# Kernel optimization log

Measured on AMD Instinct MI355X. Metric: run time of the kernel, lower is better.

The kernel has to match this reference:

```python
import jax, jax.numpy as jnp
import numpy as np

EPS = 1e-7  # keras.backend.epsilon()
ROUTINGS = 3


def _squash(s):
    # s: [B, k, d]; squash over last (capsule-dim) axis, matching squash(..., axis=-2)
    # applied to [B,1,k,d,1] in the original.
    ss = jnp.sum(s * s, axis=-1, keepdims=True) + EPS
    return (jnp.sqrt(ss) / (1.0 + ss)) * s


def setup_inputs() -> dict:
    key = jax.random.key(0)
    kx, kw, km = jax.random.split(key, 3)
    B, n, k, d = 32, 2048, 32, 16
    x = jax.random.normal(kx, (B, n, d), dtype=jnp.float32)
    # glorot-ish scale for W: fan ~ d
    W = jax.random.normal(kw, (1, n, k, d, d), dtype=jnp.float32) * (1.0 / np.sqrt(d))
    mu0 = jax.random.uniform(km, (B, k, d), dtype=jnp.float32)  # np.random.rand equivalent
    return {"x": x, "W": W, "mu0": mu0}


def reference(x, W, mu0):
    B, n, d = x.shape
    k = mu0.shape[1]
    pi = jnp.full((B, k), 1.0 / k, dtype=x.dtype)
    mu = mu0
    sigma = jnp.ones((B, k, d), dtype=x.dtype)
    log2pi = jnp.log(2.0 * jnp.pi).astype(x.dtype)
    R = jnp.zeros((B, n, k), dtype=x.dtype)
    for _ in range(ROUTINGS):
        # E-step: gamma[b,k,n] = pi_k * N(x_n | mu_k, diag(sigma_k^2)), normalized over k.
        z = (x[:, None, :, :] - mu[:, :, None, :]) / sigma[:, :, None, :]  # [B,k,n,d]
        logN = -0.5 * (jnp.sum(z * z, axis=-1) + d * log2pi) - jnp.sum(jnp.log(sigma), axis=-1)[:, :, None]
        gamma = jax.nn.softmax(jnp.log(pi)[:, :, None] + logN, axis=1)  # [B,k,n]
        R = jnp.transpose(gamma, (0, 2, 1))  # [B,n,k]
        # M-step
        N_k = jnp.sum(R, axis=1)  # [B,k]
        pi = N_k / n
        mu = jnp.einsum('bnk,bnd->bkd', R, x) / N_k[:, :, None]
        diff2 = (x[:, None, :, :] - mu[:, :, None, :]) ** 2  # [B,k,n,d]
        sigma = jnp.sqrt(jnp.einsum('bkn,bknd->bkd', gamma, diff2) / N_k[:, :, None])
    # caps_predicted[b,n,k,d] = W[0,n,k,d,:] @ x[b,n,:]
    caps_pred = jnp.einsum('nkde,bne->bnkd', W[0], x)
    s = jnp.sum(caps_pred * R[..., None], axis=1)  # [B,k,d]
    return _squash(s)
```

## Files before the change

kernel.cpp:

```cpp
#include <hip/hip_runtime.h>
#include <hip/hip_bf16.h>
#include <math.h>

#define BN 32
#define NN 2048
#define KK 32
#define DD 16
#define PART_C 16
#define PART_STRIDE 1056
#define SCAPS 256


typedef __attribute__((ext_vector_type(8))) short bf16x8;
typedef __attribute__((ext_vector_type(16))) float f32x16;

static __device__ __forceinline__ ushort f2bf(float f) {
    unsigned int u = __float_as_uint(f);
    return (ushort)((u + 0x7FFFu + ((u >> 16) & 1u)) >> 16);
}

template <int MODE, int FIRST>
static __device__ __forceinline__ void estep_body(
    int blk, const float* __restrict__ x, const float* __restrict__ mu0,
    const float* __restrict__ partIn, float* __restrict__ partOut,
    float* __restrict__ Rout) {
    const int b = blk >> 4;
    const int chunk = blk & 15;
    const int tid = threadIdx.x;
    const int wave = tid >> 6;
    const int lane = tid & 63;
    const int k = lane & 31;
    const int jj = lane >> 5;

    float mk[DD], ik[DD], ck;
    if (FIRST) {
        const float4* mp = (const float4*)(mu0 + (size_t)(b * KK + k) * DD);
#pragma unroll
        for (int q = 0; q < 4; q++) {
            float4 m4 = mp[q];
            mk[q*4+0]=m4.x; mk[q*4+1]=m4.y; mk[q*4+2]=m4.z; mk[q*4+3]=m4.w;
        }
#pragma unroll
        for (int d = 0; d < DD; d++) ik[d] = 1.0f;
        ck = -3.4657359028f;
    } else {
        float N = 0.f, sxv[DD], sxxv[DD];
#pragma unroll
        for (int d = 0; d < DD; d++) { sxv[d] = 0.f; sxxv[d] = 0.f; }
#pragma unroll
        for (int c = 0; c < PART_C; c++) {
            const float* base = partIn + (size_t)(b * PART_C + c) * PART_STRIDE;
            N += base[k];
#pragma unroll
            for (int d = 0; d < DD; d++) {
                sxv[d]  += base[(1 + d) * 32 + k];
                sxxv[d] += base[(17 + d) * 32 + k];
            }
        }
        float invN = 1.0f / N;
        float sumlog = 0.f;
#pragma unroll
        for (int d = 0; d < DD; d++) {
            float m_ = sxv[d] * invN;
            float v = fmaxf(sxxv[d] * invN - m_ * m_, 1e-12f);
            mk[d] = m_;
            ik[d] = rsqrtf(v);
            sumlog += __logf(v);
        }
        ck = __logf(N * (1.0f / NN)) - 0.5f * sumlog;
    }

    float aN = 0.f, aSx[DD], aSxx[DD];
#pragma unroll
    for (int d = 0; d < DD; d++) { aSx[d] = 0.f; aSxx[d] = 0.f; }

#pragma unroll 4
    for (int i = 0; i < 16; i++) {
        const int n = chunk * 128 + i * 8 + wave * 2 + jj;
        const float4* xp = (const float4*)(x + ((size_t)b * NN + n) * DD);
        float xv[DD];
#pragma unroll
        for (int q = 0; q < 4; q++) {
            float4 v = xp[q];
            xv[q*4+0]=v.x; xv[q*4+1]=v.y; xv[q*4+2]=v.z; xv[q*4+3]=v.w;
        }
        float qd = 0.f;
#pragma unroll
        for (int d = 0; d < DD; d++) {
            float z = (xv[d] - mk[d]) * ik[d];
            qd = fmaf(z, z, qd);
        }
        float logit = ck - 0.5f * qd;
        float m = logit;
#pragma unroll
        for (int off = 1; off < 32; off <<= 1) m = fmaxf(m, __shfl_xor(m, off));
        float e = __expf(logit - m);
        float ssum = e;
#pragma unroll
        for (int off = 1; off < 32; off <<= 1) ssum += __shfl_xor(ssum, off);
        float g = e / ssum;

        if (MODE == 1) {
            Rout[((size_t)b * NN + n) * KK + k] = g;
        } else {
            aN += g;
#pragma unroll
            for (int d = 0; d < DD; d++) {
                aSx[d] = fmaf(g, xv[d], aSx[d]);
                aSxx[d] = fmaf(g * xv[d], xv[d], aSxx[d]);
            }
        }
    }

    if (MODE == 0) {
        __shared__ float red[4][KK * 33];
        aN += __shfl_xor(aN, 32);
#pragma unroll
        for (int d = 0; d < DD; d++) {
            aSx[d] += __shfl_xor(aSx[d], 32);
            aSxx[d] += __shfl_xor(aSxx[d], 32);
        }
        if (jj == 0) {
            red[wave][k * 33 + 0] = aN;
#pragma unroll
            for (int d = 0; d < DD; d++) {
                red[wave][k * 33 + 1 + d] = aSx[d];
                red[wave][k * 33 + 17 + d] = aSxx[d];
            }
        }
        __syncthreads();
        float* outp = partOut + (size_t)(b * PART_C + chunk) * PART_STRIDE;
        for (int idx = tid; idx < KK * 33; idx += 256) {
            int kk = idx & 31, j = idx >> 5;
            float v = red[0][kk * 33 + j] + red[1][kk * 33 + j] +
                      red[2][kk * 33 + j] + red[3][kk * 33 + j];
            outp[idx] = v;
        }
    }
}

static __device__ __forceinline__ void xpack_body(int blk, const float* __restrict__ x,
                                                  ushort* __restrict__ xpk) {
    int idx = blk * 256 + threadIdx.x;
    int n = idx >> 6, l = idx & 63;
    int b = l & 31, e0 = (l >> 5) * 8;
    const float4* xp = (const float4*)(x + ((size_t)b * NN + n) * DD + e0);
    float4 a = xp[0], c = xp[1];
    ushort* o = xpk + (size_t)idx * 8;
    o[0]=f2bf(a.x); o[1]=f2bf(a.y); o[2]=f2bf(a.z); o[3]=f2bf(a.w);
    o[4]=f2bf(c.x); o[5]=f2bf(c.y); o[6]=f2bf(c.z); o[7]=f2bf(c.w);
}

__global__ __launch_bounds__(256, 4) void k_fused1(
    const float* __restrict__ x, const float* __restrict__ mu0,
    float* __restrict__ partOut, ushort* __restrict__ xpk) {
    if (blockIdx.x < 512)
        estep_body<0, 1>(blockIdx.x, x, mu0, nullptr, partOut, nullptr);
    else
        xpack_body(blockIdx.x - 512, x, xpk);
}

template <int MODE>
__global__ __launch_bounds__(256, 4) void k_estep(
    const float* __restrict__ x, const float* __restrict__ partIn,
    float* __restrict__ partOut, float* __restrict__ Rout) {
    estep_body<MODE, 0>(blockIdx.x, x, nullptr, partIn, partOut, Rout);
}

__global__ __launch_bounds__(256, 4) void k_caps(
    const float* __restrict__ W, const ushort* __restrict__ xpk,
    const float* __restrict__ R, float* __restrict__ s) {
    const int tid = threadIdx.x;
    const int wv = tid >> 6, l = tid & 63;
    const int chunk = blockIdx.x >> 2, tg = blockIdx.x & 3;
    const int t = tg * 4 + wv;
    const int col = l & 31, hi = l >> 5;
    const int kq = (l >> 4) & 1;
    float* sc = s + (size_t)chunk * (BN * KK * DD);

    float sacc[16];
#pragma unroll
    for (int q = 0; q < 16; q++) sacc[q] = 0.f;
    const f32x16 zacc = {0.f,0.f,0.f,0.f, 0.f,0.f,0.f,0.f,
                         0.f,0.f,0.f,0.f, 0.f,0.f,0.f,0.f};

#pragma unroll 4
    for (int i = 0; i < 8; i++) {
        const int n = chunk * 8 + i;
        bf16x8 af = *(const bf16x8*)(xpk + ((size_t)n * 64 + l) * 8);
        const float4* wp = (const float4*)(W + (((size_t)n * 512 + t * 32 + col) * DD) + hi * 8);
        float4 wlo = wp[0], whi = wp[1];
        bf16x8 bfr;
        bfr[0]=(short)f2bf(wlo.x); bfr[1]=(short)f2bf(wlo.y);
        bfr[2]=(short)f2bf(wlo.z); bfr[3]=(short)f2bf(wlo.w);
        bfr[4]=(short)f2bf(whi.x); bfr[5]=(short)f2bf(whi.y);
        bfr[6]=(short)f2bf(whi.z); bfr[7]=(short)f2bf(whi.w);
        const float* rn = R + (size_t)(4 * hi) * (NN * KK) + (size_t)n * KK + 2 * t + kq;
        float r0  = rn[(size_t) 0 * (NN * KK)];
        float r1  = rn[(size_t) 1 * (NN * KK)];
        float r2  = rn[(size_t) 2 * (NN * KK)];
        float r3  = rn[(size_t) 3 * (NN * KK)];
        float r4  = rn[(size_t) 8 * (NN * KK)];
        float r5  = rn[(size_t) 9 * (NN * KK)];
        float r6  = rn[(size_t)10 * (NN * KK)];
        float r7  = rn[(size_t)11 * (NN * KK)];
        float r8  = rn[(size_t)16 * (NN * KK)];
        float r9  = rn[(size_t)17 * (NN * KK)];
        float r10 = rn[(size_t)18 * (NN * KK)];
        float r11 = rn[(size_t)19 * (NN * KK)];
        float r12 = rn[(size_t)24 * (NN * KK)];
        float r13 = rn[(size_t)25 * (NN * KK)];
        float r14 = rn[(size_t)26 * (NN * KK)];
        float r15 = rn[(size_t)27 * (NN * KK)];

        f32x16 D = __builtin_amdgcn_mfma_f32_32x32x16_bf16(af, bfr, zacc, 0, 0, 0);

        sacc[0]  = fmaf(r0,  D[0],  sacc[0]);
        sacc[1]  = fmaf(r1,  D[1],  sacc[1]);
        sacc[2]  = fmaf(r2,  D[2],  sacc[2]);
        sacc[3]  = fmaf(r3,  D[3],  sacc[3]);
        sacc[4]  = fmaf(r4,  D[4],  sacc[4]);
        sacc[5]  = fmaf(r5,  D[5],  sacc[5]);
        sacc[6]  = fmaf(r6,  D[6],  sacc[6]);
        sacc[7]  = fmaf(r7,  D[7],  sacc[7]);
        sacc[8]  = fmaf(r8,  D[8],  sacc[8]);
        sacc[9]  = fmaf(r9,  D[9],  sacc[9]);
        sacc[10] = fmaf(r10, D[10], sacc[10]);
        sacc[11] = fmaf(r11, D[11], sacc[11]);
        sacc[12] = fmaf(r12, D[12], sacc[12]);
        sacc[13] = fmaf(r13, D[13], sacc[13]);
        sacc[14] = fmaf(r14, D[14], sacc[14]);
        sacc[15] = fmaf(r15, D[15], sacc[15]);
    }

    const int kd = t * 32 + col;
#pragma unroll
    for (int q = 0; q < 16; q++) {
        const int b = (q & 3) + 8 * (q >> 2) + 4 * hi;
        sc[(size_t)b * (KK * DD) + kd] = sacc[q];
    }
}

__global__ void k_squash(const float* __restrict__ s, float* __restrict__ out) {
    int idx = blockIdx.x * 256 + threadIdx.x;
    float v = 0.f;
#pragma unroll 8
    for (int c = 0; c < SCAPS; c++) v += s[(size_t)c * (BN * KK * DD) + idx];
    float ss = v * v;
#pragma unroll
    for (int off = 1; off < 16; off <<= 1) ss += __shfl_xor(ss, off);
    ss += 1e-7f;
    float scale = sqrtf(ss) / (1.0f + ss);
    out[idx] = v * scale;
}

extern "C" void kernel_launch(void* const* d_in, const int* in_sizes, int n_in,
                              void* d_out, int out_size, void* d_ws, size_t ws_size,
                              hipStream_t stream) {
    const float* x   = (const float*)d_in[0];
    const float* W   = (const float*)d_in[1];
    const float* mu0 = (const float*)d_in[2];
    float* ws    = (float*)d_ws;
    float* partA = ws;
    float* partB = ws + 540672;
    float* s     = ws + 1081344;
    float* R     = ws + 5275648;
    ushort* xpk  = (ushort*)(ws + 7372800);

    k_fused1<<<1024, 256, 0, stream>>>(x, mu0, partA, xpk);
    k_estep<0><<<512, 256, 0, stream>>>(x, partA, partB, nullptr);
    k_estep<1><<<512, 256, 0, stream>>>(x, partB, nullptr, R);
    k_caps<<<1024, 256, 0, stream>>>(W, xpk, R, s);
    k_squash<<<64, 256, 0, stream>>>(s, (float*)d_out);
}
```

Before: 100.4 us.

## Expand Gaussian quadratic form and give each caps wave two tiles

```diff
diff --git a/kernel.cpp b/kernel.cpp
--- a/kernel.cpp
+++ b/kernel.cpp
@@ -32,17 +32,19 @@
     const int k = lane & 31;
     const int jj = lane >> 5;
 
-    float mk[DD], ik[DD], ck;
+    float ak[DD], bk[DD], ck;
     if (FIRST) {
+        float msq = 0.f;
         const float4* mp = (const float4*)(mu0 + (size_t)(b * KK + k) * DD);
 #pragma unroll
         for (int q = 0; q < 4; q++) {
             float4 m4 = mp[q];
-            mk[q*4+0]=m4.x; mk[q*4+1]=m4.y; mk[q*4+2]=m4.z; mk[q*4+3]=m4.w;
-        }
-#pragma unroll
-        for (int d = 0; d < DD; d++) ik[d] = 1.0f;
-        ck = -3.4657359028f;
+            bk[q*4+0]=m4.x; bk[q*4+1]=m4.y; bk[q*4+2]=m4.z; bk[q*4+3]=m4.w;
+            msq += m4.x*m4.x + m4.y*m4.y + m4.z*m4.z + m4.w*m4.w;
+        }
+#pragma unroll
+        for (int d = 0; d < DD; d++) ak[d] = 0.5f;
+        ck = -3.4657359028f - 0.5f * msq;
     } else {
         float N = 0.f, sxv[DD], sxxv[DD];
 #pragma unroll
@@ -58,16 +60,19 @@
             }
         }
         float invN = 1.0f / N;
-        float sumlog = 0.f;
+        float sumlog = 0.f, cacc = 0.f;
 #pragma unroll
         for (int d = 0; d < DD; d++) {
             float m_ = sxv[d] * invN;
             float v = fmaxf(sxxv[d] * invN - m_ * m_, 1e-12f);
-            mk[d] = m_;
-            ik[d] = rsqrtf(v);
+            float is = rsqrtf(v);
+            float iv = is * is;
+            ak[d] = 0.5f * iv;
+            bk[d] = m_ * iv;
+            cacc = fmaf(m_ * m_, iv, cacc);
             sumlog += __logf(v);
         }
-        ck = __logf(N * (1.0f / NN)) - 0.5f * sumlog;
+        ck = __logf(N * (1.0f / NN)) - 0.5f * sumlog - 0.5f * cacc;
     }
 
     float aN = 0.f, aSx[DD], aSxx[DD];
@@ -84,13 +89,12 @@
             float4 v = xp[q];
             xv[q*4+0]=v.x; xv[q*4+1]=v.y; xv[q*4+2]=v.z; xv[q*4+3]=v.w;
         }
-        float qd = 0.f;
+        float logit = ck;
 #pragma unroll
         for (int d = 0; d < DD; d++) {
-            float z = (xv[d] - mk[d]) * ik[d];
-            qd = fmaf(z, z, qd);
-        }
-        float logit = ck - 0.5f * qd;
+            float t1 = fmaf(-ak[d], xv[d], bk[d]);
+            logit = fmaf(xv[d], t1, logit);
+        }
         float m = logit;
 #pragma unroll
         for (int off = 1; off < 32; off <<= 1) m = fmaxf(m, __shfl_xor(m, off));
@@ -172,72 +176,81 @@
     const float* __restrict__ R, float* __restrict__ s) {
     const int tid = threadIdx.x;
     const int wv = tid >> 6, l = tid & 63;
-    const int chunk = blockIdx.x >> 2, tg = blockIdx.x & 3;
-    const int t = tg * 4 + wv;
+    const int chunk = blockIdx.x >> 1, half = blockIdx.x & 1;
     const int col = l & 31, hi = l >> 5;
     const int kq = (l >> 4) & 1;
     float* sc = s + (size_t)chunk * (BN * KK * DD);
 
-    float sacc[16];
-#pragma unroll
-    for (int q = 0; q < 16; q++) sacc[q] = 0.f;
+    float sacc[2][16];
+#pragma unroll
+    for (int ii = 0; ii < 2; ii++)
+#pragma unroll
+        for (int q = 0; q < 16; q++) sacc[ii][q] = 0.f;
     const f32x16 zacc = {0.f,0.f,0.f,0.f, 0.f,0.f,0.f,0.f,
                          0.f,0.f,0.f,0.f, 0.f,0.f,0.f,0.f};
 
-#pragma unroll 4
+#pragma unroll 2
     for (int i = 0; i < 8; i++) {
         const int n = chunk * 8 + i;
         bf16x8 af = *(const bf16x8*)(xpk + ((size_t)n * 64 + l) * 8);
-        const float4* wp = (const float4*)(W + (((size_t)n * 512 + t * 32 + col) * DD) + hi * 8);
-        float4 wlo = wp[0], whi = wp[1];
-        bf16x8 bfr;
-        bfr[0]=(short)f2bf(wlo.x); bfr[1]=(short)f2bf(wlo.y);
-        bfr[2]=(short)f2bf(wlo.z); bfr[3]=(short)f2bf(wlo.w);
-        bfr[4]=(short)f2bf(whi.x); bfr[5]=(short)f2bf(whi.y);
-        bfr[6]=(short)f2bf(whi.z); bfr[7]=(short)f2bf(whi.w);
-        const float* rn = R + (size_t)(4 * hi) * (NN * KK) + (size_t)n * KK + 2 * t + kq;
-        float r0  = rn[(size_t) 0 * (NN * KK)];
-        float r1  = rn[(size_t) 1 * (NN * KK)];
-        float r2  = rn[(size_t) 2 * (NN * KK)];
-        float r3  = rn[(size_t) 3 * (NN * KK)];
-        float r4  = rn[(size_t) 8 * (NN * KK)];
-        float r5  = rn[(size_t) 9 * (NN * KK)];
-        float r6  = rn[(size_t)10 * (NN * KK)];
-        float r7  = rn[(size_t)11 * (NN * KK)];
-        float r8  = rn[(size_t)16 * (NN * KK)];
-        float r9  = rn[(size_t)17 * (NN * KK)];
-        float r10 = rn[(size_t)18 * (NN * KK)];
-        float r11 = rn[(size_t)19 * (NN * KK)];
-        float r12 = rn[(size_t)24 * (NN * KK)];
-        float r13 = rn[(size_t)25 * (NN * KK)];
-        float r14 = rn[(size_t)26 * (NN * KK)];
-        float r15 = rn[(size_t)27 * (NN * KK)];
-
-        f32x16 D = __builtin_amdgcn_mfma_f32_32x32x16_bf16(af, bfr, zacc, 0, 0, 0);
-
-        sacc[0]  = fmaf(r0,  D[0],  sacc[0]);
-        sacc[1]  = fmaf(r1,  D[1],  sacc[1]);
-        sacc[2]  = fmaf(r2,  D[2],  sacc[2]);
-        sacc[3]  = fmaf(r3,  D[3],  sacc[3]);
-        sacc[4]  = fmaf(r4,  D[4],  sacc[4]);
-        sacc[5]  = fmaf(r5,  D[5],  sacc[5]);
-        sacc[6]  = fmaf(r6,  D[6],  sacc[6]);
-        sacc[7]  = fmaf(r7,  D[7],  sacc[7]);
-        sacc[8]  = fmaf(r8,  D[8],  sacc[8]);
-        sacc[9]  = fmaf(r9,  D[9],  sacc[9]);
-        sacc[10] = fmaf(r10, D[10], sacc[10]);
-        sacc[11] = fmaf(r11, D[11], sacc[11]);
-        sacc[12] = fmaf(r12, D[12], sacc[12]);
-        sacc[13] = fmaf(r13, D[13], sacc[13]);
-        sacc[14] = fmaf(r14, D[14], sacc[14]);
-        sacc[15] = fmaf(r15, D[15], sacc[15]);
-    }
-
-    const int kd = t * 32 + col;
-#pragma unroll
-    for (int q = 0; q < 16; q++) {
-        const int b = (q & 3) + 8 * (q >> 2) + 4 * hi;
-        sc[(size_t)b * (KK * DD) + kd] = sacc[q];
+#pragma unroll
+        for (int ii = 0; ii < 2; ii++) {
+            const int t = half * 8 + wv * 2 + ii;
+            const float4* wp = (const float4*)(W + (((size_t)n * 512 + t * 32 + col) * DD) + hi * 8);
+            float4 wlo = wp[0], whi = wp[1];
+            bf16x8 bfr;
+            bfr[0]=(short)f2bf(wlo.x); bfr[1]=(short)f2bf(wlo.y);
+            bfr[2]=(short)f2bf(wlo.z); bfr[3]=(short)f2bf(wlo.w);
+            bfr[4]=(short)f2bf(whi.x); bfr[5]=(short)f2bf(whi.y);
+            bfr[6]=(short)f2bf(whi.z); bfr[7]=(short)f2bf(whi.w);
+            const float* rn = R + (size_t)(4 * hi) * (NN * KK) + (size_t)n * KK + 2 * t + kq;
+            float r0  = rn[(size_t) 0 * (NN * KK)];
+            float r1  = rn[(size_t) 1 * (NN * KK)];
+            float r2  = rn[(size_t) 2 * (NN * KK)];
+            float r3  = rn[(size_t) 3 * (NN * KK)];
+            float r4  = rn[(size_t) 8 * (NN * KK)];
+            float r5  = rn[(size_t) 9 * (NN * KK)];
+            float r6  = rn[(size_t)10 * (NN * KK)];
+            float r7  = rn[(size_t)11 * (NN * KK)];
+            float r8  = rn[(size_t)16 * (NN * KK)];
+            float r9  = rn[(size_t)17 * (NN * KK)];
+            float r10 = rn[(size_t)18 * (NN * KK)];
+            float r11 = rn[(size_t)19 * (NN * KK)];
+            float r12 = rn[(size_t)24 * (NN * KK)];
+            float r13 = rn[(size_t)25 * (NN * KK)];
+            float r14 = rn[(size_t)26 * (NN * KK)];
+            float r15 = rn[(size_t)27 * (NN * KK)];
+
+            f32x16 D = __builtin_amdgcn_mfma_f32_32x32x16_bf16(af, bfr, zacc, 0, 0, 0);
+
+            sacc[ii][0]  = fmaf(r0,  D[0],  sacc[ii][0]);
+            sacc[ii][1]  = fmaf(r1,  D[1],  sacc[ii][1]);
+            sacc[ii][2]  = fmaf(r2,  D[2],  sacc[ii][2]);
+            sacc[ii][3]  = fmaf(r3,  D[3],  sacc[ii][3]);
+            sacc[ii][4]  = fmaf(r4,  D[4],  sacc[ii][4]);
+            sacc[ii][5]  = fmaf(r5,  D[5],  sacc[ii][5]);
+            sacc[ii][6]  = fmaf(r6,  D[6],  sacc[ii][6]);
+            sacc[ii][7]  = fmaf(r7,  D[7],  sacc[ii][7]);
+            sacc[ii][8]  = fmaf(r8,  D[8],  sacc[ii][8]);
+            sacc[ii][9]  = fmaf(r9,  D[9],  sacc[ii][9]);
+            sacc[ii][10] = fmaf(r10, D[10], sacc[ii][10]);
+            sacc[ii][11] = fmaf(r11, D[11], sacc[ii][11]);
+            sacc[ii][12] = fmaf(r12, D[12], sacc[ii][12]);
+            sacc[ii][13] = fmaf(r13, D[13], sacc[ii][13]);
+            sacc[ii][14] = fmaf(r14, D[14], sacc[ii][14]);
+            sacc[ii][15] = fmaf(r15, D[15], sacc[ii][15]);
+        }
+    }
+
+#pragma unroll
+    for (int ii = 0; ii < 2; ii++) {
+        const int t = half * 8 + wv * 2 + ii;
+        const int kd = t * 32 + col;
+#pragma unroll
+        for (int q = 0; q < 16; q++) {
+            const int b = (q & 3) + 8 * (q >> 2) + 4 * hi;
+            sc[(size_t)b * (KK * DD) + kd] = sacc[ii][q];
+        }
     }
 }
 
@@ -270,6 +283,6 @@
     k_fused1<<<1024, 256, 0, stream>>>(x, mu0, partA, xpk);
     k_estep<0><<<512, 256, 0, stream>>>(x, partA, partB, nullptr);
     k_estep<1><<<512, 256, 0, stream>>>(x, partB, nullptr, R);
-    k_caps<<<1024, 256, 0, stream>>>(W, xpk, R, s);
+    k_caps<<<512, 256, 0, stream>>>(W, xpk, R, s);
     k_squash<<<64, 256, 0, stream>>>(s, (float*)d_out);
 }
```

Result: slower. 107.8 us (+7.4%).
